# Kernel tuning notes

Hardware: AMD Instinct MI355X
Metric: run time of the kernel (lower is better)

## Reference

```python
import jax, jax.numpy as jnp
import numpy as np

N = 8192      # number of samples (x.shape[0])
D = 64        # out_feat / spectral embedding dim
K_NN = 32     # config['school']['k']
KP1 = 64      # columns in idx (>= K_NN + 1)
N_PROJ_ITERS = 100  # Newton iterations for simplex projection


def setup_inputs() -> dict:
    key = jax.random.key(0)
    k1, k2, k3, k4 = jax.random.split(key, 4)
    Y = jax.random.normal(k1, (N, D), jnp.float32)
    semantic_H = jax.random.normal(k2, (N, D), jnp.float32)
    ortho_H = jax.random.normal(k3, (N, D), jnp.float32)
    idx = jax.random.randint(k4, (N, KP1), 0, N)
    return {"Y": Y, "semantic_H": semantic_H, "ortho_H": ortho_H,
            "idx": idx, "alpha": 1, "beta": 1}


def eproj_simplex_rows(v, k=1.0):
    """Project each row of v onto the simplex {x >= 0, sum(x) = k}.
    Fixed-iteration Newton solve for the Lagrange multiplier (matches the
    iterative EProjSimplex_new_matrix; it is a fixed point once converged)."""
    n = v.shape[1]
    v0 = v - v.mean(axis=1, keepdims=True) + k / n   # shift so sum(v0) = k per row

    def body(_, lam):
        v1 = v0 - lam[:, None]
        pos = v1 > 0
        npos = jnp.maximum(pos.sum(axis=1), 1)       # -g
        f = jnp.where(pos, v1, 0.0).sum(axis=1) - k  # constraint residual
        return lam + f / npos                         # lam - f/g

    lam = jax.lax.fori_loop(0, N_PROJ_ITERS, body,
                            jnp.zeros(v.shape[0], v.dtype))
    return jnp.maximum(v0 - lam[:, None], 0.0)


def reference(Y, semantic_H, ortho_H, idx, alpha, beta):
    num = Y.shape[0]
    idxa0 = idx[:, 1:K_NN + 1]                                   # [N, k]
    # kNN gather + pairwise L2 distances (O(N*k*d), no dense NxN distances)
    dfi = jnp.sqrt(((Y[:, None, :] - Y[idxa0]) ** 2).sum(-1) + 1e-8)          # [N, k]
    dxi = jnp.sqrt(((ortho_H[:, None, :] - ortho_H[idxa0]) ** 2).sum(-1) + 1e-8)
    ad = -(dxi + beta * dfi) / (2 * alpha)
    w = eproj_simplex_rows(ad)                                   # [N, k] simplex weights
    # scatter into dense NxN adjacency (faithful to A.scatter_(1, idxa0, w))
    rows = jnp.arange(num)[:, None]
    A = jnp.zeros((num, num), Y.dtype).at[rows, idxa0].set(w)
    embs_hom = A @ semantic_H                                    # [N, D]
    return embs_hom, A, Y
```

## Files before the change

kernel.cpp:

```cpp
#include <hip/hip_runtime.h>

#define NROWS 8192
#define DDIM  64
#define KNN   32
#define MAXIT 100

__device__ __forceinline__ float scalar_val(const void* p) {
    int iv = *(const int*)p;
    if (iv > -1000000 && iv < 1000000) return (float)iv;
    return *(const float*)p;
}

__global__ __launch_bounds__(256, 4) void school_fused_kernel(
    const float* __restrict__ Y,
    const float* __restrict__ semH,
    const float* __restrict__ orthoH,
    const int*   __restrict__ idx,
    const void*  alpha_p,
    const void*  beta_p,
    float* __restrict__ embs,
    float* __restrict__ A,
    float* __restrict__ Yout)
{
    __shared__ int   col_s[8][KNN];
    __shared__ float w_s[8][KNN];
    __shared__ float ad_s[8][KNN];

    const int tid  = threadIdx.x;
    const int j    = tid & 31;
    const int r    = tid >> 5;
    const int row0 = blockIdx.x * 8;
    const int row  = row0 + r;

    const float alpha = scalar_val(alpha_p);
    const float beta  = scalar_val(beta_p);

    const int col = idx[row * 64 + 1 + j];
    col_s[r][j] = col;

    const float4* Y4 = (const float4*)Y;
    const float4* O4 = (const float4*)orthoH;
    const int q = j & 15;
    const float4 ownY = Y4[(size_t)row * 16 + q];
    const float4 ownO = O4[(size_t)row * 16 + q];

    #pragma unroll 4
    for (int t = 0; t < 16; ++t) {
        const int c = col_s[r][2 * t + (j >> 4)];
        const float4 gY = Y4[(size_t)c * 16 + q];
        const float4 gO = O4[(size_t)c * 16 + q];
        float ex = ownY.x - gY.x, ey = ownY.y - gY.y,
              ez = ownY.z - gY.z, ew = ownY.w - gY.w;
        float dY = ex * ex + ey * ey + ez * ez + ew * ew;
        ex = ownO.x - gO.x; ey = ownO.y - gO.y;
        ez = ownO.z - gO.z; ew = ownO.w - gO.w;
        float dO = ex * ex + ey * ey + ez * ez + ew * ew;
        #pragma unroll
        for (int m = 1; m <= 8; m <<= 1) {
            dY += __shfl_xor(dY, m, 64);
            dO += __shfl_xor(dO, m, 64);
        }
        if ((j & 15) == 0) {
            float dfv = sqrtf(dY + 1e-8f);
            float dxv = sqrtf(dO + 1e-8f);
            ad_s[r][2 * t + (j >> 4)] = -(dxv + beta * dfv) / (2.f * alpha);
        }
    }
    const float ad = ad_s[r][j];

    float s = ad;
    #pragma unroll
    for (int m = 1; m <= 16; m <<= 1) s += __shfl_xor(s, m, 64);
    const float v0 = ad - s * (1.f / 32.f) + (1.f / 32.f);

    float lam = 0.f;
    #pragma unroll 1
    for (int it = 0; it < MAXIT; ++it) {
        float v1 = v0 - lam;
        float p = v1 > 0.f ? v1 : 0.f;
        float c = v1 > 0.f ? 1.f : 0.f;
        #pragma unroll
        for (int m = 1; m <= 16; m <<= 1) {
            p += __shfl_xor(p, m, 64);
            c += __shfl_xor(c, m, 64);
        }
        float step = (p - 1.f) / fmaxf(c, 1.f);
        lam += step;
        if (__all(fabsf(step) <= 1e-6f ? 1 : 0)) break;
    }
    const float w = fmaxf(v0 - lam, 0.f);

    bool dead = false;
    for (int jj = j + 1; jj < 32; ++jj)
        dead |= (col_s[r][jj] == col);
    w_s[r][j] = dead ? 0.f : w;

    {
        float2 acc = make_float2(0.f, 0.f);
        const float2* H2 = (const float2*)semH;
        #pragma unroll 4
        for (int jj = 0; jj < KNN; ++jj) {
            float wv = w_s[r][jj];
            int   c  = col_s[r][jj];
            float2 h = H2[(size_t)c * 32 + j];
            acc.x += wv * h.x;
            acc.y += wv * h.y;
        }
        ((float2*)embs)[(size_t)row * 32 + j] = acc;
    }

    {
        const float2* Y2 = (const float2*)(Y + (size_t)row0 * DDIM);
        float2* O2 = (float2*)(Yout + (size_t)row0 * DDIM);
        O2[tid] = Y2[tid];
    }

    unsigned k0 = 0xFFFFFFFFu, k1 = 0xFFFFFFFFu, k2 = 0xFFFFFFFFu, k3 = 0xFFFFFFFFu;
    float f0 = 0.f, f1 = 0.f, f2 = 0.f, f3 = 0.f;
    int nhit = 0;
    #pragma unroll 1
    for (int jj = 0; jj < 32; ++jj) {
        int c = col_s[r][jj];
        if (((c >> 2) & 31) == j) {
            unsigned key = ((unsigned)(c >> 7) << 2) | (unsigned)(c & 3);
            float wv = w_s[r][jj];
            k3 = (nhit == 3) ? key : k3;  f3 = (nhit == 3) ? wv : f3;
            k2 = (nhit == 2) ? key : k2;  f2 = (nhit == 2) ? wv : f2;
            k1 = (nhit == 1) ? key : k1;  f1 = (nhit == 1) ? wv : f1;
            k0 = (nhit == 0) ? key : k0;  f0 = (nhit == 0) ? wv : f0;
            nhit++;
        }
    }

    {
        float4* Arow4 = (float4*)(A + (size_t)row * NROWS);
        #pragma unroll 4
        for (int ss = 0; ss < 64; ++ss) {
            float4 v = make_float4(0.f, 0.f, 0.f, 0.f);
            #define APPLY_SLOT(kk, ff)                                   \
                if ((kk >> 2) == (unsigned)ss) {                         \
                    int p_ = (int)(kk & 3u);                             \
                    v.x = (p_ == 0) ? ff : v.x;                          \
                    v.y = (p_ == 1) ? ff : v.y;                          \
                    v.z = (p_ == 2) ? ff : v.z;                          \
                    v.w = (p_ == 3) ? ff : v.w;                          \
                }
            APPLY_SLOT(k0, f0)
            APPLY_SLOT(k1, f1)
            APPLY_SLOT(k2, f2)
            APPLY_SLOT(k3, f3)
            #undef APPLY_SLOT
            Arow4[(ss << 5) + j] = v;
        }
    }

    if (nhit > 4) {
        asm volatile("s_waitcnt vmcnt(0)" ::: "memory");
        int cnt = 0;
        for (int jj = 0; jj < 32; ++jj) {
            int c = col_s[r][jj];
            if (((c >> 2) & 31) == j) {
                if (cnt >= 4) {
                    A[(size_t)row * NROWS + c] = w_s[r][jj];
                    asm volatile("s_waitcnt vmcnt(0)" ::: "memory");
                }
                cnt++;
            }
        }
    }
}

extern "C" void kernel_launch(void* const* d_in, const int* in_sizes, int n_in,
                              void* d_out, int out_size, void* d_ws, size_t ws_size,
                              hipStream_t stream) {
    const float* Y      = (const float*)d_in[0];
    const float* semH   = (const float*)d_in[1];
    const float* orthoH = (const float*)d_in[2];
    const int*   idx    = (const int*)d_in[3];
    const void*  alpha  = d_in[4];
    const void*  beta   = d_in[5];

    float* out  = (float*)d_out;
    float* embs = out;
    float* A    = out + (size_t)NROWS * DDIM;
    float* Yout = A + (size_t)NROWS * NROWS;

    school_fused_kernel<<<NROWS / 8, 256, 0, stream>>>(
        Y, semH, orthoH, idx, alpha, beta, embs, A, Yout);
}
```

Before: 63.49 us.

## Issue zero stores for A before the simplex solve, write hit slots afterwards

The code builds a per-lane bitmask of which float4 slots of the A row hold kNN entries. It then writes zeros to all other slots right after the distance computation, before the Newton projection loop, so the dense 256MB write stream overlaps the latency-bound iteration. After the solve, only the masked slots get their weights. The embedding gather and Y copy move to the end of the kernel. The data-dependent while loop adds divergence, and the early stores may compete with the gathers for memory bandwidth.

```diff
diff --git a/kernel.cpp b/kernel.cpp
--- a/kernel.cpp
+++ b/kernel.cpp
@@ -38,6 +38,13 @@
     const int col = idx[row * 64 + 1 + j];
     col_s[r][j] = col;
 
+    unsigned long long hitmask = 0ull;
+    #pragma unroll 1
+    for (int jj = 0; jj < 32; ++jj) {
+        int c = col_s[r][jj];
+        if (((c >> 2) & 31) == j) hitmask |= 1ull << (c >> 7);
+    }
+
     const float4* Y4 = (const float4*)Y;
     const float4* O4 = (const float4*)orthoH;
     const int q = j & 15;
@@ -56,9 +63,9 @@
         ez = ownO.z - gO.z; ew = ownO.w - gO.w;
         float dO = ex * ex + ey * ey + ez * ez + ew * ew;
         #pragma unroll
-        for (int m = 1; m <= 8; m <<= 1) {
-            dY += __shfl_xor(dY, m, 64);
-            dO += __shfl_xor(dO, m, 64);
+        for (int mm = 1; mm <= 8; mm <<= 1) {
+            dY += __shfl_xor(dY, mm, 64);
+            dO += __shfl_xor(dO, mm, 64);
         }
         if ((j & 15) == 0) {
             float dfv = sqrtf(dY + 1e-8f);
@@ -68,9 +75,23 @@
     }
     const float ad = ad_s[r][j];
 
+    __builtin_amdgcn_sched_barrier(0);
+
+    {
+        const float4 z4 = make_float4(0.f, 0.f, 0.f, 0.f);
+        float4* Arow4 = (float4*)(A + (size_t)row * NROWS);
+        #pragma unroll 8
+        for (int ss = 0; ss < 64; ++ss) {
+            if (!((hitmask >> ss) & 1ull))
+                Arow4[(ss << 5) + j] = z4;
+        }
+    }
+
+    __builtin_amdgcn_sched_barrier(0);
+
     float s = ad;
     #pragma unroll
-    for (int m = 1; m <= 16; m <<= 1) s += __shfl_xor(s, m, 64);
+    for (int mm = 1; mm <= 16; mm <<= 1) s += __shfl_xor(s, mm, 64);
     const float v0 = ad - s * (1.f / 32.f) + (1.f / 32.f);
 
     float lam = 0.f;
@@ -80,9 +101,9 @@
         float p = v1 > 0.f ? v1 : 0.f;
         float c = v1 > 0.f ? 1.f : 0.f;
         #pragma unroll
-        for (int m = 1; m <= 16; m <<= 1) {
-            p += __shfl_xor(p, m, 64);
-            c += __shfl_xor(c, m, 64);
+        for (int mm = 1; mm <= 16; mm <<= 1) {
+            p += __shfl_xor(p, mm, 64);
+            c += __shfl_xor(c, mm, 64);
         }
         float step = (p - 1.f) / fmaxf(c, 1.f);
         lam += step;
@@ -94,26 +115,6 @@
     for (int jj = j + 1; jj < 32; ++jj)
         dead |= (col_s[r][jj] == col);
     w_s[r][j] = dead ? 0.f : w;
-
-    {
-        float2 acc = make_float2(0.f, 0.f);
-        const float2* H2 = (const float2*)semH;
-        #pragma unroll 4
-        for (int jj = 0; jj < KNN; ++jj) {
-            float wv = w_s[r][jj];
-            int   c  = col_s[r][jj];
-            float2 h = H2[(size_t)c * 32 + j];
-            acc.x += wv * h.x;
-            acc.y += wv * h.y;
-        }
-        ((float2*)embs)[(size_t)row * 32 + j] = acc;
-    }
-
-    {
-        const float2* Y2 = (const float2*)(Y + (size_t)row0 * DDIM);
-        float2* O2 = (float2*)(Yout + (size_t)row0 * DDIM);
-        O2[tid] = Y2[tid];
-    }
 
     unsigned k0 = 0xFFFFFFFFu, k1 = 0xFFFFFFFFu, k2 = 0xFFFFFFFFu, k3 = 0xFFFFFFFFu;
     float f0 = 0.f, f1 = 0.f, f2 = 0.f, f3 = 0.f;
@@ -134,11 +135,13 @@
 
     {
         float4* Arow4 = (float4*)(A + (size_t)row * NROWS);
-        #pragma unroll 4
-        for (int ss = 0; ss < 64; ++ss) {
+        unsigned long long mrem = hitmask;
+        while (mrem) {
+            int ss = __ffsll((unsigned long long)mrem) - 1;
+            mrem &= mrem - 1;
             float4 v = make_float4(0.f, 0.f, 0.f, 0.f);
             #define APPLY_SLOT(kk, ff)                                   \
-                if ((kk >> 2) == (unsigned)ss) {                         \
+                if ((int)(kk >> 2) == ss) {                              \
                     int p_ = (int)(kk & 3u);                             \
                     v.x = (p_ == 0) ? ff : v.x;                          \
                     v.y = (p_ == 1) ? ff : v.y;                          \
@@ -168,6 +171,26 @@
             }
         }
     }
+
+    {
+        float2 acc = make_float2(0.f, 0.f);
+        const float2* H2 = (const float2*)semH;
+        #pragma unroll 4
+        for (int jj = 0; jj < KNN; ++jj) {
+            float wv = w_s[r][jj];
+            int   c  = col_s[r][jj];
+            float2 h = H2[(size_t)c * 32 + j];
+            acc.x += wv * h.x;
+            acc.y += wv * h.y;
+        }
+        ((float2*)embs)[(size_t)row * 32 + j] = acc;
+    }
+
+    {
+        const float2* Y2 = (const float2*)(Y + (size_t)row0 * DDIM);
+        float2* O2 = (float2*)(Yout + (size_t)row0 * DDIM);
+        O2[tid] = Y2[tid];
+    }
 }
 
 extern "C" void kernel_launch(void* const* d_in, const int* in_sizes, int n_in,
```

New measurement: 69.25 us. +9.1%, slower.
